# Kernel optimization log

Hardware: AMD Instinct MI355X
Metric: run time of the kernel (lower is better)

The kernel has to match this reference:

```python
import jax, jax.numpy as jnp
import numpy as np
import math

HIDDEN = 2048
HEADS = 16
HEAD_DIM = HIDDEN // HEADS
MAX_SEQ = 2048
BATCH = 2
SEQ = 2048


def _rope_tables(seq_len, dim):
    inv_freq = 1.0 / (10000.0 ** (np.arange(0, dim, 2, dtype=np.float32) / dim))
    t = np.arange(seq_len, dtype=np.float32)
    freqs = np.einsum('i,j->ij', t, inv_freq)  # [S, dim/2]
    emb = np.concatenate([freqs, freqs], axis=-1)  # [S, dim]
    return jnp.asarray(np.cos(emb)), jnp.asarray(np.sin(emb))


def setup_inputs() -> dict:
    key = jax.random.key(0)
    ks = jax.random.split(key, 5)
    s = 1.0 / math.sqrt(HIDDEN)
    x = jax.random.normal(ks[0], (BATCH, SEQ, HIDDEN), dtype=jnp.float32)
    Wq = jax.random.normal(ks[1], (HIDDEN, HIDDEN), dtype=jnp.float32) * s
    Wk = jax.random.normal(ks[2], (HIDDEN, HIDDEN), dtype=jnp.float32) * s
    Wv = jax.random.normal(ks[3], (HIDDEN, HIDDEN), dtype=jnp.float32) * s
    Wo = jax.random.normal(ks[4], (HIDDEN, HIDDEN), dtype=jnp.float32) * s
    return {"x": x, "Wq": Wq, "Wk": Wk, "Wv": Wv, "Wo": Wo}


def _rotate_half(t):
    t1, t2 = t[..., : t.shape[-1] // 2], t[..., t.shape[-1] // 2 :]
    return jnp.concatenate([-t2, t1], axis=-1)


def reference(x, Wq, Wk, Wv, Wo):
    b, s, _ = x.shape
    # nn.Linear: y = x @ W.T
    def proj(W):
        return jnp.einsum('bsd,hd->bsh', x, W).reshape(b, s, HEADS, HEAD_DIM).transpose(0, 2, 1, 3)
    q, k, v = proj(Wq), proj(Wk), proj(Wv)  # [b, H, s, hd]
    cos, sin = _rope_tables(s, HEAD_DIM)    # [s, hd]
    cos = cos[None, None]
    sin = sin[None, None]
    q = q * cos + _rotate_half(q) * sin
    k = k * cos + _rotate_half(k) * sin
    scale = 1.0 / math.sqrt(HEAD_DIM)
    scores = jnp.einsum('bhqd,bhkd->bhqk', q, k) * scale
    causal = jnp.triu(jnp.ones((s, s), dtype=bool), k=1)
    scores = jnp.where(causal[None, None], -jnp.inf, scores)
    attn = jax.nn.softmax(scores, axis=-1)
    out = jnp.einsum('bhqk,bhkd->bhqd', attn, v)
    out = out.transpose(0, 2, 1, 3).reshape(b, s, HIDDEN)
    return jnp.einsum('bsd,hd->bsh', out, Wo)
```

## Files before the change

### kernel.cpp

```cpp
#include <hip/hip_runtime.h>
#include <stdint.h>


#define SCALE_Q 0.08838834764831845f

typedef short bf16x8 __attribute__((ext_vector_type(8)));
typedef float f32x4 __attribute__((ext_vector_type(4)));
typedef unsigned short u16x4v __attribute__((ext_vector_type(4)));
typedef unsigned short u16x8v __attribute__((ext_vector_type(8)));

__device__ __forceinline__ unsigned short f2bf(float f) {
  unsigned u = __float_as_uint(f);
  return (unsigned short)((u + 0x7FFFu + ((u >> 16) & 1u)) >> 16);
}
__device__ __forceinline__ float bf2f(unsigned short h) {
  return __uint_as_float(((unsigned)h) << 16);
}
__device__ __forceinline__ void gld16(void* lds, const void* g) {
  __builtin_amdgcn_global_load_lds(
      (const __attribute__((address_space(1))) unsigned int*)g,
      (__attribute__((address_space(3))) unsigned int*)lds, 16, 0, 0);
}

__global__ __launch_bounds__(256) void cvt_all(
    const float* __restrict__ x, const float* __restrict__ wq,
    const float* __restrict__ wk, const float* __restrict__ wv,
    const float* __restrict__ wo,
    unsigned short* __restrict__ xb, unsigned short* __restrict__ wqkv,
    unsigned short* __restrict__ wob) {
  int r = blockIdx.y;
  size_t i = ((size_t)blockIdx.x * 256 + threadIdx.x) * 8;
  const float* src; unsigned short* dst; size_t n;
  if (r == 0)      { src = x;  dst = xb;             n = 8388608; }
  else if (r == 1) { src = wq; dst = wqkv;           n = 4194304; }
  else if (r == 2) { src = wk; dst = wqkv + 4194304; n = 4194304; }
  else if (r == 3) { src = wv; dst = wqkv + 8388608; n = 4194304; }
  else             { src = wo; dst = wob;            n = 4194304; }
  if (i >= n) return;
  float4 a = *(const float4*)(src + i);
  float4 b = *(const float4*)(src + i + 4);
  u16x8v o;
  o[0] = f2bf(a.x); o[1] = f2bf(a.y); o[2] = f2bf(a.z); o[3] = f2bf(a.w);
  o[4] = f2bf(b.x); o[5] = f2bf(b.y); o[6] = f2bf(b.z); o[7] = f2bf(b.w);
  *(u16x8v*)(dst + i) = o;
}

__global__ __launch_bounds__(256) void rope_table(float* __restrict__ ct, float* __restrict__ st) {
  int id = blockIdx.x * 256 + threadIdx.x;
  int s = id >> 6, j = id & 63;
  float inv = __powf(10000.0f, -(float)j * (1.0f / 64.0f));
  float a = (float)s * inv;
  ct[id] = __cosf(a);
  st[id] = __sinf(a);
}

template <int MODE>
__global__ __launch_bounds__(512, 2) void gemm8p(
    const unsigned short* __restrict__ A, const unsigned short* __restrict__ B,
    void* __restrict__ C0, void* __restrict__ C1, void* __restrict__ C2,
    int N, int Kd, int nbx) {
  __shared__ unsigned short As[4][128 * 64];
  __shared__ unsigned short Bs[4][128 * 64];
  const int t = threadIdx.x;
  const int lane = t & 63, w = t >> 6;
  const int g = lane >> 4, c15 = lane & 15;
  const int wm = w >> 2, wn = w & 3;

  const int chunk = (int)blockIdx.x & 7;
  const int idx = (int)blockIdx.x >> 3;
  const int cpc = nbx >> 3;
  const int row = idx & 15;
  const int col = chunk * cpc + (idx >> 4);
  const int brow = row * 256, bcol = col * 256;

  const int l = t >> 3;
  const int lg = (t & 7) ^ (l & 7);
  const unsigned short* srcA = A + (size_t)(brow + l + ((lg >> 2) << 7)) * Kd + (lg & 3) * 8;
  const unsigned short* srcB = B + (size_t)(bcol + l + ((lg >> 2) << 7)) * Kd + (lg & 3) * 8;

  auto stage = [&](int kt) {
    const int buf = kt & 3;
    const unsigned short* a = srcA + kt * 32;
    const unsigned short* b = srcB + kt * 32;
    gld16((char*)As[buf] + t * 16, a);
    gld16((char*)As[buf] + 8192 + t * 16, a + (size_t)64 * Kd);
    gld16((char*)Bs[buf] + t * 16, b);
    gld16((char*)Bs[buf] + 8192 + t * 16, b + (size_t)64 * Kd);
  };

  const int aoff = c15 * 128 + ((((wm << 2) | g) ^ (c15 & 7)) << 4);
  const int boff = ((wn & 1) << 13) + c15 * 128 + (((((wn >> 1) << 2) | g) ^ (c15 & 7)) << 4);

  f32x4 zero4 = {0.f, 0.f, 0.f, 0.f};
  f32x4 acc[8][4];
#pragma unroll
  for (int a_ = 0; a_ < 8; ++a_)
#pragma unroll
    for (int b_ = 0; b_ < 4; ++b_) acc[a_][b_] = zero4;

  const int nk = Kd >> 5;
  stage(0); stage(1); stage(2);
  asm volatile("s_waitcnt vmcnt(8)" ::: "memory");
  __builtin_amdgcn_s_barrier();

  for (int kt = 0; kt < nk; ++kt) {
    const char* ab = (const char*)As[kt & 3];
    const char* bb = (const char*)Bs[kt & 3];
    bf16x8 bfv[4], af0[4], af1[4];
#pragma unroll
    for (int nj = 0; nj < 4; ++nj) bfv[nj] = *(const bf16x8*)(bb + boff + nj * 2048);
#pragma unroll
    for (int mi = 0; mi < 4; ++mi) af0[mi] = *(const bf16x8*)(ab + aoff + mi * 2048);
    __builtin_amdgcn_sched_barrier(0);
#pragma unroll
    for (int mi = 0; mi < 4; ++mi) af1[mi] = *(const bf16x8*)(ab + aoff + (mi + 4) * 2048);
    if (kt + 3 < nk) stage(kt + 3);
    asm volatile("s_waitcnt lgkmcnt(4)" ::: "memory");
    __builtin_amdgcn_sched_barrier(0);
    __builtin_amdgcn_s_setprio(1);
#pragma unroll
    for (int mi = 0; mi < 4; ++mi)
#pragma unroll
      for (int nj = 0; nj < 4; ++nj)
        acc[mi][nj] = __builtin_amdgcn_mfma_f32_16x16x32_bf16(
            af0[mi], bfv[nj], acc[mi][nj], 0, 0, 0);
    __builtin_amdgcn_s_setprio(0);
    asm volatile("s_waitcnt lgkmcnt(0)" ::: "memory");
    __builtin_amdgcn_sched_barrier(0);
    __builtin_amdgcn_s_setprio(1);
#pragma unroll
    for (int mi = 0; mi < 4; ++mi)
#pragma unroll
      for (int nj = 0; nj < 4; ++nj)
        acc[mi + 4][nj] = __builtin_amdgcn_mfma_f32_16x16x32_bf16(
            af1[mi], bfv[nj], acc[mi + 4][nj], 0, 0, 0);
    __builtin_amdgcn_s_setprio(0);
    if (kt + 3 < nk) {
      asm volatile("s_waitcnt vmcnt(8)" ::: "memory");
    } else if (kt + 2 < nk) {
      asm volatile("s_waitcnt vmcnt(4)" ::: "memory");
    } else if (kt + 1 < nk) {
      asm volatile("s_waitcnt vmcnt(0)" ::: "memory");
    }
    __builtin_amdgcn_s_barrier();
  }

#pragma unroll
  for (int mi = 0; mi < 8; ++mi) {
#pragma unroll
    for (int nj = 0; nj < 4; ++nj) {
      f32x4 v = acc[mi][nj];
      int row0 = brow + wm * 128 + mi * 16 + g * 4;
      int colc = bcol + wn * 64 + nj * 16 + c15;
      if (MODE == 0) {
        int which = colc >> 11;
        int hc = colc & 2047;
        int bh = ((row0 >> 11) << 4) + (hc >> 7);
        int d = hc & 127, s0 = row0 & 2047;
        if (which == 2) {
          u16x4v pk;
          pk[0] = f2bf(v[0]); pk[1] = f2bf(v[1]); pk[2] = f2bf(v[2]); pk[3] = f2bf(v[3]);
          *(u16x4v*)((unsigned short*)C2 + ((size_t)bh * 128 + d) * 2048 + s0) = pk;
        } else {
          unsigned short* dst =
              (unsigned short*)(which ? C1 : C0) + ((size_t)bh * 2048 + s0) * 128 + d;
#pragma unroll
          for (int i = 0; i < 4; ++i) dst[(size_t)i * 128] = f2bf(v[i]);
        }
      } else {
        float* Cf = (float*)C0;
#pragma unroll
        for (int i = 0; i < 4; ++i) Cf[(size_t)(row0 + i) * N + colc] = v[i];
      }
    }
  }
}

__global__ __launch_bounds__(256) void rope_apply(
    unsigned short* __restrict__ Q, unsigned short* __restrict__ K,
    const float* __restrict__ ct, const float* __restrict__ st) {
  int id = blockIdx.x * 256 + threadIdx.x;
  int o = id & 7;
  int s = (id >> 3) & 2047;
  int bh = id >> 14;
  size_t base = ((size_t)bh * 2048 + s) * 128 + o * 8;
  u16x8v qlo = *(u16x8v*)(Q + base), qhi = *(u16x8v*)(Q + base + 64);
  u16x8v klo = *(u16x8v*)(K + base), khi = *(u16x8v*)(K + base + 64);
  const float* cp = ct + s * 64 + o * 8;
  const float* sp = st + s * 64 + o * 8;
#pragma unroll
  for (int j = 0; j < 8; ++j) {
    float c = cp[j], sn = sp[j];
    float ql = bf2f(qlo[j]), qh = bf2f(qhi[j]);
    qlo[j] = f2bf((ql * c - qh * sn) * SCALE_Q);
    qhi[j] = f2bf((qh * c + ql * sn) * SCALE_Q);
    float kl = bf2f(klo[j]), kh = bf2f(khi[j]);
    klo[j] = f2bf(kl * c - kh * sn);
    khi[j] = f2bf(kh * c + kl * sn);
  }
  *(u16x8v*)(Q + base) = qlo; *(u16x8v*)(Q + base + 64) = qhi;
  *(u16x8v*)(K + base) = klo; *(u16x8v*)(K + base + 64) = khi;
}

__global__ __launch_bounds__(256) void attn_fwd(
    const unsigned short* __restrict__ Qg, const unsigned short* __restrict__ Kg,
    const unsigned short* __restrict__ Vtg, unsigned short* __restrict__ Og) {
  __shared__ unsigned short Ks[2][64 * 128];
  __shared__ unsigned short Vs[2][64 * 128];
  __shared__ unsigned short Pl[4][16 * 88];
  const int t = threadIdx.x;
  const int lane = t & 63, w = t >> 6;
  const int g = lane >> 4, c15 = lane & 15;
  const int pair = blockIdx.x;
  const int bh = blockIdx.y;
  const int b = bh >> 4, h = bh & 15;

  const int ksrow = t >> 4;
  const int kssl = (t & 15) ^ ksrow;
  const unsigned short* kp = Kg + ((size_t)bh * 2048 + ksrow) * 128 + kssl * 8;
  const int vsrow = t >> 3;
  const int vssl = (t & 7) ^ (vsrow & 7);
  const unsigned short* vp = Vtg + ((size_t)bh * 128 + vsrow) * 2048 + vssl * 8;

  auto stageTile = [&](int buf, int tkv) {
#pragma unroll
    for (int c = 0; c < 4; ++c) {
      gld16((char*)Ks[buf] + c * 4096 + t * 16, kp + (size_t)(tkv * 64 + c * 16) * 128);
      gld16((char*)Vs[buf] + c * 4096 + t * 16, vp + (size_t)c * 32 * 2048 + tkv * 64);
    }
  };

  f32x4 zero4 = {0.f, 0.f, 0.f, 0.f};
  f32x4 o[8];
  float mrow[4], lrow[4];
  bf16x8 qf[4];

  auto computeTile = [&](int buf, int qb, int tkv) {
    const int q0 = qb * 64;
    const int qrow = q0 + w * 16;
    f32x4 sv[4];
    __builtin_amdgcn_s_setprio(1);
#pragma unroll
    for (int cb = 0; cb < 4; ++cb) {
      f32x4 z = zero4;
#pragma unroll
      for (int kf = 0; kf < 4; ++kf) {
        int row = cb * 16 + c15;
        int p = (kf * 4 + g) ^ c15;
        bf16x8 kfr = *(const bf16x8*)((const char*)Ks[buf] + row * 256 + p * 16);
        z = __builtin_amdgcn_mfma_f32_16x16x32_bf16(qf[kf], kfr, z, 0, 0, 0);
      }
      sv[cb] = z;
    }
    __builtin_amdgcn_s_setprio(0);
    if (tkv == qb) {
#pragma unroll
      for (int cb = 0; cb < 4; ++cb)
#pragma unroll
        for (int i = 0; i < 4; ++i) {
          int colk = q0 + cb * 16 + c15;
          int rq = qrow + g * 4 + i;
          if (colk > rq) sv[cb][i] = -1e30f;
        }
    }
    float pmx[4];
#pragma unroll
    for (int i = 0; i < 4; ++i)
      pmx[i] = fmaxf(fmaxf(sv[0][i], sv[1][i]), fmaxf(sv[2][i], sv[3][i]));
#pragma unroll
    for (int dd = 1; dd < 16; dd <<= 1)
#pragma unroll
      for (int i = 0; i < 4; ++i) pmx[i] = fmaxf(pmx[i], __shfl_xor(pmx[i], dd));
    float sc[4], psum[4];
#pragma unroll
    for (int i = 0; i < 4; ++i) {
      float nm = fmaxf(mrow[i], pmx[i]);
      sc[i] = __expf(mrow[i] - nm);
      mrow[i] = nm;
      psum[i] = 0.f;
    }
#pragma unroll
    for (int cb = 0; cb < 4; ++cb)
#pragma unroll
      for (int i = 0; i < 4; ++i) {
        float e = __expf(sv[cb][i] - mrow[i]);
        sv[cb][i] = e;
        psum[i] += e;
      }
#pragma unroll
    for (int dd = 1; dd < 16; dd <<= 1)
#pragma unroll
      for (int i = 0; i < 4; ++i) psum[i] += __shfl_xor(psum[i], dd);
#pragma unroll
    for (int i = 0; i < 4; ++i) lrow[i] = lrow[i] * sc[i] + psum[i];
#pragma unroll
    for (int db = 0; db < 8; ++db)
#pragma unroll
      for (int i = 0; i < 4; ++i) o[db][i] *= sc[i];

    unsigned short* pw = &Pl[w][0];
#pragma unroll
    for (int cb = 0; cb < 4; ++cb)
#pragma unroll
      for (int i = 0; i < 4; ++i)
        pw[(g * 4 + i) * 88 + cb * 16 + c15] = f2bf(sv[cb][i]);
    bf16x8 pf[2];
#pragma unroll
    for (int kb = 0; kb < 2; ++kb)
      pf[kb] = *(const bf16x8*)((const char*)pw + c15 * 176 + kb * 64 + g * 16);

    __builtin_amdgcn_s_setprio(1);
#pragma unroll
    for (int db = 0; db < 8; ++db) {
#pragma unroll
      for (int kb = 0; kb < 2; ++kb) {
        int row = db * 16 + c15;
        int p = (kb * 4 + g) ^ (c15 & 7);
        bf16x8 vfr = *(const bf16x8*)((const char*)Vs[buf] + row * 128 + p * 16);
        o[db] = __builtin_amdgcn_mfma_f32_16x16x32_bf16(pf[kb], vfr, o[db], 0, 0, 0);
      }
    }
    __builtin_amdgcn_s_setprio(0);
  };

  auto loadQ = [&](int qb) {
    const unsigned short* qp = Qg + ((size_t)bh * 2048 + qb * 64 + w * 16 + c15) * 128 + g * 8;
#pragma unroll
    for (int kf = 0; kf < 4; ++kf) qf[kf] = *(const bf16x8*)(qp + kf * 32);
#pragma unroll
    for (int db = 0; db < 8; ++db) o[db] = zero4;
#pragma unroll
    for (int i = 0; i < 4; ++i) { mrow[i] = -1e30f; lrow[i] = 0.f; }
  };

  auto writeO = [&](int qb) {
    float linv[4];
#pragma unroll
    for (int i = 0; i < 4; ++i) linv[i] = 1.0f / lrow[i];
#pragma unroll
    for (int db = 0; db < 8; ++db)
#pragma unroll
      for (int i = 0; i < 4; ++i) {
        int q = qb * 64 + w * 16 + g * 4 + i;
        Og[((size_t)(b * 2048 + q)) * 2048 + h * 128 + db * 16 + c15] =
            f2bf(o[db][i] * linv[i]);
      }
  };

  const int qbA = pair, qbB = 31 - pair;
  const int ntA = qbA + 1, ntB = qbB + 1;
  int cur = 0;

  stageTile(0, 0);
  loadQ(qbA);
  for (int tkv = 0; tkv < ntA; ++tkv) {
    __syncthreads();
    if (tkv + 1 < ntA) stageTile(cur ^ 1, tkv + 1);
    else               stageTile(cur ^ 1, 0);
    computeTile(cur, qbA, tkv);
    cur ^= 1;
  }
  writeO(qbA);
  loadQ(qbB);
  for (int tkv = 0; tkv < ntB; ++tkv) {
    __syncthreads();
    if (tkv + 1 < ntB) stageTile(cur ^ 1, tkv + 1);
    computeTile(cur, qbB, tkv);
    cur ^= 1;
  }
  writeO(qbB);
}

extern "C" void kernel_launch(void* const* d_in, const int* in_sizes, int n_in,
                              void* d_out, int out_size, void* d_ws, size_t ws_size,
                              hipStream_t stream) {
  const float* x  = (const float*)d_in[0];
  const float* Wq = (const float*)d_in[1];
  const float* Wk = (const float*)d_in[2];
  const float* Wv = (const float*)d_in[3];
  const float* Wo = (const float*)d_in[4];
  char* p = (char*)d_ws;
  unsigned short* xb    = (unsigned short*)p;
  unsigned short* wqkvb = (unsigned short*)(p + 16777216);
  unsigned short* wob   = (unsigned short*)(p + 41943040);
  unsigned short* Qb    = (unsigned short*)(p + 50331648);
  unsigned short* Kb    = (unsigned short*)(p + 67108864);
  unsigned short* Vt    = (unsigned short*)(p + 83886080);
  float* ctab           = (float*)(p + 100663296);
  float* stab           = (float*)(p + 101187584);
  unsigned short* Ao = xb;

  cvt_all<<<dim3(4096, 5), 256, 0, stream>>>(x, Wq, Wk, Wv, Wo, xb, wqkvb, wob);
  rope_table<<<512, 256, 0, stream>>>(ctab, stab);
  gemm8p<0><<<384, 512, 0, stream>>>(xb, wqkvb, Qb, Kb, Vt, 6144, 2048, 24);
  rope_apply<<<2048, 256, 0, stream>>>(Qb, Kb, ctab, stab);
  attn_fwd<<<dim3(16, 32), 256, 0, stream>>>(Qb, Kb, Vt, Ao);
  gemm8p<1><<<128, 512, 0, stream>>>(Ao, wob, d_out, nullptr, nullptr, 2048, 2048, 8);
}
```

Measured before the change: 303.5 us.

## Restructure GEMM into double-buffered K=64 ping-pong pipeline with interleaved staging

Replaces the 4-stage K=32 LDS ring in the projection GEMMs with a 2-buffer K=64 scheme. Global-to-LDS loads are split into quarter-tile components that are issued between MFMA clusters, with barriers and priority toggles fencing each phase. The goal is to hide global-load and LDS-read latency behind matrix math with fewer loop iterations. The cost is many extra workgroup barriers per iteration and tighter buffer reuse, which could stall warps. The remaining edits only rename variables and add macros.

Result: slower. 318.6 us (+5.0%).

```diff
diff --git a/kernel.cpp b/kernel.cpp
--- a/kernel.cpp
+++ b/kernel.cpp
@@ -21,6 +21,14 @@
       (const __attribute__((address_space(1))) unsigned int*)g,
       (__attribute__((address_space(3))) unsigned int*)lds, 16, 0, 0);
 }
+
+#define BAR __builtin_amdgcn_s_barrier()
+#define SB0 __builtin_amdgcn_sched_barrier(0)
+#define LGKM0 asm volatile("s_waitcnt lgkmcnt(0)" ::: "memory")
+#define VM4 asm volatile("s_waitcnt vmcnt(4)" ::: "memory")
+#define VM0 asm volatile("s_waitcnt vmcnt(0)" ::: "memory")
+#define PRIO1 __builtin_amdgcn_s_setprio(1)
+#define PRIO0 __builtin_amdgcn_s_setprio(0)
 
 __global__ __launch_bounds__(256) void cvt_all(
     const float* __restrict__ x, const float* __restrict__ wq,
@@ -55,12 +63,12 @@
 }
 
 template <int MODE>
-__global__ __launch_bounds__(512, 2) void gemm8p(
+__global__ __launch_bounds__(512, 2) void gemm_m2(
     const unsigned short* __restrict__ A, const unsigned short* __restrict__ B,
     void* __restrict__ C0, void* __restrict__ C1, void* __restrict__ C2,
     int N, int Kd, int nbx) {
-  __shared__ unsigned short As[4][128 * 64];
-  __shared__ unsigned short Bs[4][128 * 64];
+  __shared__ unsigned short As[2][256 * 64];
+  __shared__ unsigned short Bs[2][256 * 64];
   const int t = threadIdx.x;
   const int lane = t & 63, w = t >> 6;
   const int g = lane >> 4, c15 = lane & 15;
@@ -73,23 +81,27 @@
   const int col = chunk * cpc + (idx >> 4);
   const int brow = row * 256, bcol = col * 256;
 
-  const int l = t >> 3;
-  const int lg = (t & 7) ^ (l & 7);
-  const unsigned short* srcA = A + (size_t)(brow + l + ((lg >> 2) << 7)) * Kd + (lg & 3) * 8;
-  const unsigned short* srcB = B + (size_t)(bcol + l + ((lg >> 2) << 7)) * Kd + (lg & 3) * 8;
-
-  auto stage = [&](int kt) {
-    const int buf = kt & 3;
-    const unsigned short* a = srcA + kt * 32;
-    const unsigned short* b = srcB + kt * 32;
-    gld16((char*)As[buf] + t * 16, a);
-    gld16((char*)As[buf] + 8192 + t * 16, a + (size_t)64 * Kd);
-    gld16((char*)Bs[buf] + t * 16, b);
-    gld16((char*)Bs[buf] + 8192 + t * 16, b + (size_t)64 * Kd);
-  };
-
-  const int aoff = c15 * 128 + ((((wm << 2) | g) ^ (c15 & 7)) << 4);
-  const int boff = ((wn & 1) << 13) + c15 * 128 + (((((wn >> 1) << 2) | g) ^ (c15 & 7)) << 4);
+  const int r8 = t >> 3;
+  const int lg = (t & 7) ^ (r8 & 7);
+  const unsigned short* srcA = A + (size_t)(brow + r8) * Kd + lg * 8;
+  const unsigned short* srcB = B + (size_t)(bcol + r8) * Kd + lg * 8;
+
+  const int nk = Kd >> 6;
+  const int nit = nk >> 1;
+
+  auto stage = [&](int step, int comp) {
+    if (step >= nk) return;
+    char* dst = ((comp & 2) ? (char*)Bs[step & 1] : (char*)As[step & 1]) + (comp & 1) * 16384;
+    const unsigned short* src =
+        ((comp & 2) ? srcB : srcA) + (size_t)((comp & 1) * 128) * Kd + step * 64;
+    gld16(dst + t * 16, src);
+    gld16(dst + 8192 + t * 16, src + (size_t)64 * Kd);
+  };
+
+  const int aBase = (wm * 128 + c15) * 128;
+  const int bBase = (wn * 64 + c15) * 128;
+  const int sl0 = ((g) ^ (c15 & 7)) * 16;
+  const int sl1 = ((4 + g) ^ (c15 & 7)) * 16;
 
   f32x4 zero4 = {0.f, 0.f, 0.f, 0.f};
   f32x4 acc[8][4];
@@ -98,51 +110,66 @@
 #pragma unroll
     for (int b_ = 0; b_ < 4; ++b_) acc[a_][b_] = zero4;
 
-  const int nk = Kd >> 5;
-  stage(0); stage(1); stage(2);
-  asm volatile("s_waitcnt vmcnt(8)" ::: "memory");
-  __builtin_amdgcn_s_barrier();
-
-  for (int kt = 0; kt < nk; ++kt) {
-    const char* ab = (const char*)As[kt & 3];
-    const char* bb = (const char*)Bs[kt & 3];
-    bf16x8 bfv[4], af0[4], af1[4];
-#pragma unroll
-    for (int nj = 0; nj < 4; ++nj) bfv[nj] = *(const bf16x8*)(bb + boff + nj * 2048);
-#pragma unroll
-    for (int mi = 0; mi < 4; ++mi) af0[mi] = *(const bf16x8*)(ab + aoff + mi * 2048);
-    __builtin_amdgcn_sched_barrier(0);
-#pragma unroll
-    for (int mi = 0; mi < 4; ++mi) af1[mi] = *(const bf16x8*)(ab + aoff + (mi + 4) * 2048);
-    if (kt + 3 < nk) stage(kt + 3);
-    asm volatile("s_waitcnt lgkmcnt(4)" ::: "memory");
-    __builtin_amdgcn_sched_barrier(0);
-    __builtin_amdgcn_s_setprio(1);
+  bf16x8 af0[8], bf0[4], af1[8], bf1[4];
+
+  auto RD = [&](const char* ab, const char* bb, bf16x8* AF, bf16x8* BF, int sl) {
+#pragma unroll
+    for (int mi = 0; mi < 8; ++mi) AF[mi] = *(const bf16x8*)(ab + aBase + mi * 2048 + sl);
+#pragma unroll
+    for (int nj = 0; nj < 4; ++nj) BF[nj] = *(const bf16x8*)(bb + bBase + nj * 2048 + sl);
+  };
+  auto MF16 = [&](const bf16x8* AF, const bf16x8* BF, int mb) {
 #pragma unroll
     for (int mi = 0; mi < 4; ++mi)
 #pragma unroll
       for (int nj = 0; nj < 4; ++nj)
-        acc[mi][nj] = __builtin_amdgcn_mfma_f32_16x16x32_bf16(
-            af0[mi], bfv[nj], acc[mi][nj], 0, 0, 0);
-    __builtin_amdgcn_s_setprio(0);
-    asm volatile("s_waitcnt lgkmcnt(0)" ::: "memory");
-    __builtin_amdgcn_sched_barrier(0);
-    __builtin_amdgcn_s_setprio(1);
-#pragma unroll
-    for (int mi = 0; mi < 4; ++mi)
-#pragma unroll
-      for (int nj = 0; nj < 4; ++nj)
-        acc[mi + 4][nj] = __builtin_amdgcn_mfma_f32_16x16x32_bf16(
-            af1[mi], bfv[nj], acc[mi + 4][nj], 0, 0, 0);
-    __builtin_amdgcn_s_setprio(0);
-    if (kt + 3 < nk) {
-      asm volatile("s_waitcnt vmcnt(8)" ::: "memory");
-    } else if (kt + 2 < nk) {
-      asm volatile("s_waitcnt vmcnt(4)" ::: "memory");
-    } else if (kt + 1 < nk) {
-      asm volatile("s_waitcnt vmcnt(0)" ::: "memory");
-    }
-    __builtin_amdgcn_s_barrier();
+        acc[mb + mi][nj] = __builtin_amdgcn_mfma_f32_16x16x32_bf16(
+            AF[mb + mi], BF[nj], acc[mb + mi][nj], 0, 0, 0);
+  };
+
+  stage(0, 0); stage(0, 1); stage(0, 2); stage(0, 3);
+  stage(1, 0); stage(1, 1);
+  VM4;
+  BAR; SB0;
+
+  for (int i = 0; i < nit; ++i) {
+    const char* a0 = (const char*)As[0]; const char* b0 = (const char*)Bs[0];
+    const char* a1 = (const char*)As[1]; const char* b1 = (const char*)Bs[1];
+    const int sB = 2 * i + 1, sN = 2 * i + 2, sN1 = 2 * i + 3;
+    RD(a0, b0, af0, bf0, sl0); stage(sB, 2);
+    BAR; LGKM0; SB0;
+    PRIO1; MF16(af0, bf0, 0); PRIO0;
+    BAR; SB0;
+    RD(a0, b0, af1, bf1, sl1); stage(sB, 3);
+    BAR; LGKM0; SB0;
+    PRIO1; MF16(af0, bf0, 4); PRIO0;
+    BAR; SB0;
+    stage(sN, 0);
+    BAR; SB0;
+    PRIO1; MF16(af1, bf1, 0); PRIO0;
+    BAR; SB0;
+    stage(sN, 1);
+    BAR; SB0;
+    PRIO1; MF16(af1, bf1, 4); PRIO0;
+    if (i + 1 == nit) { VM0; } else { VM4; }
+    BAR; SB0;
+    RD(a1, b1, af0, bf0, sl0); stage(sN, 2);
+    BAR; LGKM0; SB0;
+    PRIO1; MF16(af0, bf0, 0); PRIO0;
+    BAR; SB0;
+    RD(a1, b1, af1, bf1, sl1); stage(sN, 3);
+    BAR; LGKM0; SB0;
+    PRIO1; MF16(af0, bf0, 4); PRIO0;
+    BAR; SB0;
+    stage(sN1, 0);
+    BAR; SB0;
+    PRIO1; MF16(af1, bf1, 0); PRIO0;
+    BAR; SB0;
+    stage(sN1, 1);
+    BAR; SB0;
+    PRIO1; MF16(af1, bf1, 4); PRIO0;
+    VM4;
+    BAR; SB0;
   }
 
 #pragma unroll
@@ -165,12 +192,12 @@
           unsigned short* dst =
               (unsigned short*)(which ? C1 : C0) + ((size_t)bh * 2048 + s0) * 128 + d;
 #pragma unroll
-          for (int i = 0; i < 4; ++i) dst[(size_t)i * 128] = f2bf(v[i]);
+          for (int i2 = 0; i2 < 4; ++i2) dst[(size_t)i2 * 128] = f2bf(v[i2]);
         }
       } else {
         float* Cf = (float*)C0;
 #pragma unroll
-        for (int i = 0; i < 4; ++i) Cf[(size_t)(row0 + i) * N + colc] = v[i];
+        for (int i2 = 0; i2 < 4; ++i2) Cf[(size_t)(row0 + i2) * N + colc] = v[i2];
       }
     }
   }
@@ -239,20 +266,20 @@
     const int q0 = qb * 64;
     const int qrow = q0 + w * 16;
     f32x4 sv[4];
-    __builtin_amdgcn_s_setprio(1);
+    PRIO1;
 #pragma unroll
     for (int cb = 0; cb < 4; ++cb) {
       f32x4 z = zero4;
 #pragma unroll
       for (int kf = 0; kf < 4; ++kf) {
-        int row = cb * 16 + c15;
+        int rowk = cb * 16 + c15;
         int p = (kf * 4 + g) ^ c15;
-        bf16x8 kfr = *(const bf16x8*)((const char*)Ks[buf] + row * 256 + p * 16);
+        bf16x8 kfr = *(const bf16x8*)((const char*)Ks[buf] + rowk * 256 + p * 16);
         z = __builtin_amdgcn_mfma_f32_16x16x32_bf16(qf[kf], kfr, z, 0, 0, 0);
       }
       sv[cb] = z;
     }
-    __builtin_amdgcn_s_setprio(0);
+    PRIO0;
     if (tkv == qb) {
 #pragma unroll
       for (int cb = 0; cb < 4; ++cb)
@@ -309,18 +336,18 @@
     for (int kb = 0; kb < 2; ++kb)
       pf[kb] = *(const bf16x8*)((const char*)pw + c15 * 176 + kb * 64 + g * 16);
 
-    __builtin_amdgcn_s_setprio(1);
+    PRIO1;
 #pragma unroll
     for (int db = 0; db < 8; ++db) {
 #pragma unroll
       for (int kb = 0; kb < 2; ++kb) {
-        int row = db * 16 + c15;
+        int rowv = db * 16 + c15;
         int p = (kb * 4 + g) ^ (c15 & 7);
-        bf16x8 vfr = *(const bf16x8*)((const char*)Vs[buf] + row * 128 + p * 16);
+        bf16x8 vfr = *(const bf16x8*)((const char*)Vs[buf] + rowv * 128 + p * 16);
         o[db] = __builtin_amdgcn_mfma_f32_16x16x32_bf16(pf[kb], vfr, o[db], 0, 0, 0);
       }
     }
-    __builtin_amdgcn_s_setprio(0);
+    PRIO0;
   };
 
   auto loadQ = [&](int qb) {
@@ -392,8 +419,8 @@
 
   cvt_all<<<dim3(4096, 5), 256, 0, stream>>>(x, Wq, Wk, Wv, Wo, xb, wqkvb, wob);
   rope_table<<<512, 256, 0, stream>>>(ctab, stab);
-  gemm8p<0><<<384, 512, 0, stream>>>(xb, wqkvb, Qb, Kb, Vt, 6144, 2048, 24);
+  gemm_m2<0><<<384, 512, 0, stream>>>(xb, wqkvb, Qb, Kb, Vt, 6144, 2048, 24);
   rope_apply<<<2048, 256, 0, stream>>>(Qb, Kb, ctab, stab);
   attn_fwd<<<dim3(16, 32), 256, 0, stream>>>(Qb, Kb, Vt, Ao);
-  gemm8p<1><<<128, 512, 0, stream>>>(Ao, wob, d_out, nullptr, nullptr, 2048, 2048, 8);
-}
+  gemm_m2<1><<<128, 512, 0, stream>>>(Ao, wob, d_out, nullptr, nullptr, 2048, 2048, 8);
+}
```

## Shrink QKV GEMM to double buffering and use simpler 128x128 GEMM for output

Applied to the files above, without the earlier changes.

The QKV projection GEMM goes from a 4-stage to a 2-stage LDS pipeline, prefetching one tile ahead with a full vmcnt(0) wait each iteration. Halving LDS use may allow more resident blocks. The output projection now runs in a new single-buffered 128x128-tile kernel with 256 threads and 512 blocks instead of 128 large 256x256 blocks, meant to improve CU occupancy on that smaller GEMM. The cost is less latency hiding: loads are no longer overlapped with compute in the new kernel, and the QKV GEMM has a shallower prefetch.

Result: faster. 297.1 us (-2.1%).

```diff
diff --git a/kernel.cpp b/kernel.cpp
--- a/kernel.cpp
+++ b/kernel.cpp
@@ -54,13 +54,12 @@
   st[id] = __sinf(a);
 }
 
-template <int MODE>
-__global__ __launch_bounds__(512, 2) void gemm8p(
+__global__ __launch_bounds__(512, 2) void gemm8p2(
     const unsigned short* __restrict__ A, const unsigned short* __restrict__ B,
     void* __restrict__ C0, void* __restrict__ C1, void* __restrict__ C2,
     int N, int Kd, int nbx) {
-  __shared__ unsigned short As[4][128 * 64];
-  __shared__ unsigned short Bs[4][128 * 64];
+  __shared__ unsigned short As[2][128 * 64];
+  __shared__ unsigned short Bs[2][128 * 64];
   const int t = threadIdx.x;
   const int lane = t & 63, w = t >> 6;
   const int g = lane >> 4, c15 = lane & 15;
@@ -79,7 +78,7 @@
   const unsigned short* srcB = B + (size_t)(bcol + l + ((lg >> 2) << 7)) * Kd + (lg & 3) * 8;
 
   auto stage = [&](int kt) {
-    const int buf = kt & 3;
+    const int buf = kt & 1;
     const unsigned short* a = srcA + kt * 32;
     const unsigned short* b = srcB + kt * 32;
     gld16((char*)As[buf] + t * 16, a);
@@ -99,13 +98,13 @@
     for (int b_ = 0; b_ < 4; ++b_) acc[a_][b_] = zero4;
 
   const int nk = Kd >> 5;
-  stage(0); stage(1); stage(2);
-  asm volatile("s_waitcnt vmcnt(8)" ::: "memory");
+  stage(0);
+  asm volatile("s_waitcnt vmcnt(0)" ::: "memory");
   __builtin_amdgcn_s_barrier();
 
   for (int kt = 0; kt < nk; ++kt) {
-    const char* ab = (const char*)As[kt & 3];
-    const char* bb = (const char*)Bs[kt & 3];
+    const char* ab = (const char*)As[kt & 1];
+    const char* bb = (const char*)Bs[kt & 1];
     bf16x8 bfv[4], af0[4], af1[4];
 #pragma unroll
     for (int nj = 0; nj < 4; ++nj) bfv[nj] = *(const bf16x8*)(bb + boff + nj * 2048);
@@ -114,7 +113,7 @@
     __builtin_amdgcn_sched_barrier(0);
 #pragma unroll
     for (int mi = 0; mi < 4; ++mi) af1[mi] = *(const bf16x8*)(ab + aoff + (mi + 4) * 2048);
-    if (kt + 3 < nk) stage(kt + 3);
+    if (kt + 1 < nk) stage(kt + 1);
     asm volatile("s_waitcnt lgkmcnt(4)" ::: "memory");
     __builtin_amdgcn_sched_barrier(0);
     __builtin_amdgcn_s_setprio(1);
@@ -135,13 +134,7 @@
         acc[mi + 4][nj] = __builtin_amdgcn_mfma_f32_16x16x32_bf16(
             af1[mi], bfv[nj], acc[mi + 4][nj], 0, 0, 0);
     __builtin_amdgcn_s_setprio(0);
-    if (kt + 3 < nk) {
-      asm volatile("s_waitcnt vmcnt(8)" ::: "memory");
-    } else if (kt + 2 < nk) {
-      asm volatile("s_waitcnt vmcnt(4)" ::: "memory");
-    } else if (kt + 1 < nk) {
-      asm volatile("s_waitcnt vmcnt(0)" ::: "memory");
-    }
+    asm volatile("s_waitcnt vmcnt(0)" ::: "memory");
     __builtin_amdgcn_s_barrier();
   }
 
@@ -152,28 +145,95 @@
       f32x4 v = acc[mi][nj];
       int row0 = brow + wm * 128 + mi * 16 + g * 4;
       int colc = bcol + wn * 64 + nj * 16 + c15;
-      if (MODE == 0) {
-        int which = colc >> 11;
-        int hc = colc & 2047;
-        int bh = ((row0 >> 11) << 4) + (hc >> 7);
-        int d = hc & 127, s0 = row0 & 2047;
-        if (which == 2) {
-          u16x4v pk;
-          pk[0] = f2bf(v[0]); pk[1] = f2bf(v[1]); pk[2] = f2bf(v[2]); pk[3] = f2bf(v[3]);
-          *(u16x4v*)((unsigned short*)C2 + ((size_t)bh * 128 + d) * 2048 + s0) = pk;
-        } else {
-          unsigned short* dst =
-              (unsigned short*)(which ? C1 : C0) + ((size_t)bh * 2048 + s0) * 128 + d;
-#pragma unroll
-          for (int i = 0; i < 4; ++i) dst[(size_t)i * 128] = f2bf(v[i]);
-        }
+      int which = colc >> 11;
+      int hc = colc & 2047;
+      int bh = ((row0 >> 11) << 4) + (hc >> 7);
+      int d = hc & 127, s0 = row0 & 2047;
+      if (which == 2) {
+        u16x4v pk;
+        pk[0] = f2bf(v[0]); pk[1] = f2bf(v[1]); pk[2] = f2bf(v[2]); pk[3] = f2bf(v[3]);
+        *(u16x4v*)((unsigned short*)C2 + ((size_t)bh * 128 + d) * 2048 + s0) = pk;
       } else {
-        float* Cf = (float*)C0;
-#pragma unroll
-        for (int i = 0; i < 4; ++i) Cf[(size_t)(row0 + i) * N + colc] = v[i];
-      }
-    }
-  }
+        unsigned short* dst =
+            (unsigned short*)(which ? C1 : C0) + ((size_t)bh * 2048 + s0) * 128 + d;
+#pragma unroll
+        for (int i2 = 0; i2 < 4; ++i2) dst[(size_t)i2 * 128] = f2bf(v[i2]);
+      }
+    }
+  }
+}
+
+__global__ __launch_bounds__(256) void gemm_bt(
+    const unsigned short* __restrict__ A, const unsigned short* __restrict__ B,
+    float* __restrict__ C, int N, int Kd) {
+  __shared__ unsigned short As[128 * 64];
+  __shared__ unsigned short Bs[128 * 64];
+  const int t = threadIdx.x;
+  const int lane = t & 63, w = t >> 6;
+  const int g = lane >> 4, c15 = lane & 15;
+  const int wr = w >> 1, wc = w & 1;
+  const int brow = blockIdx.y * 128, bcol = blockIdx.x * 128;
+  const int srow = t >> 3;
+  const int ssl = (t & 7) ^ (srow & 7);
+  const unsigned short* pA = A + (size_t)(brow + srow) * Kd + ssl * 8;
+  const unsigned short* pB = B + (size_t)(bcol + srow) * Kd + ssl * 8;
+
+  int aoff[4][2], boff[4][2];
+#pragma unroll
+  for (int mi = 0; mi < 4; ++mi)
+#pragma unroll
+    for (int kk = 0; kk < 2; ++kk) {
+      int arow = wr * 64 + mi * 16 + c15;
+      int bcolr = wc * 64 + mi * 16 + c15;
+      int p = (kk * 4 + g) ^ (c15 & 7);
+      aoff[mi][kk] = arow * 128 + (p << 4);
+      boff[mi][kk] = bcolr * 128 + (p << 4);
+    }
+  f32x4 zero4 = {0.f, 0.f, 0.f, 0.f};
+  f32x4 acc[4][4];
+#pragma unroll
+  for (int a_ = 0; a_ < 4; ++a_)
+#pragma unroll
+    for (int b_ = 0; b_ < 4; ++b_) acc[a_][b_] = zero4;
+
+  const int nk = Kd >> 6;
+  for (int kt = 0; kt < nk; ++kt) {
+    const unsigned short* a0 = pA + kt * 64;
+    const unsigned short* b0 = pB + kt * 64;
+#pragma unroll
+    for (int c = 0; c < 4; ++c) {
+      gld16((char*)As + c * 4096 + t * 16, a0 + (size_t)c * 32 * Kd);
+      gld16((char*)Bs + c * 4096 + t * 16, b0 + (size_t)c * 32 * Kd);
+    }
+    __syncthreads();
+    bf16x8 af[4][2], bfv[4][2];
+#pragma unroll
+    for (int mi = 0; mi < 4; ++mi)
+#pragma unroll
+      for (int kk = 0; kk < 2; ++kk) {
+        af[mi][kk] = *(const bf16x8*)((const char*)As + aoff[mi][kk]);
+        bfv[mi][kk] = *(const bf16x8*)((const char*)Bs + boff[mi][kk]);
+      }
+#pragma unroll
+    for (int mi = 0; mi < 4; ++mi)
+#pragma unroll
+      for (int nj = 0; nj < 4; ++nj)
+#pragma unroll
+        for (int kk = 0; kk < 2; ++kk)
+          acc[mi][nj] = __builtin_amdgcn_mfma_f32_16x16x32_bf16(
+              af[mi][kk], bfv[nj][kk], acc[mi][nj], 0, 0, 0);
+    __syncthreads();
+  }
+#pragma unroll
+  for (int mi = 0; mi < 4; ++mi)
+#pragma unroll
+    for (int nj = 0; nj < 4; ++nj) {
+      f32x4 v = acc[mi][nj];
+      int row0 = brow + wr * 64 + mi * 16 + g * 4;
+      int colc = bcol + wc * 64 + nj * 16 + c15;
+#pragma unroll
+      for (int i = 0; i < 4; ++i) C[(size_t)(row0 + i) * N + colc] = v[i];
+    }
 }
 
 __global__ __launch_bounds__(256) void rope_apply(
@@ -245,9 +305,9 @@
       f32x4 z = zero4;
 #pragma unroll
       for (int kf = 0; kf < 4; ++kf) {
-        int row = cb * 16 + c15;
+        int rowk = cb * 16 + c15;
         int p = (kf * 4 + g) ^ c15;
-        bf16x8 kfr = *(const bf16x8*)((const char*)Ks[buf] + row * 256 + p * 16);
+        bf16x8 kfr = *(const bf16x8*)((const char*)Ks[buf] + rowk * 256 + p * 16);
         z = __builtin_amdgcn_mfma_f32_16x16x32_bf16(qf[kf], kfr, z, 0, 0, 0);
       }
       sv[cb] = z;
@@ -314,9 +374,9 @@
     for (int db = 0; db < 8; ++db) {
 #pragma unroll
       for (int kb = 0; kb < 2; ++kb) {
-        int row = db * 16 + c15;
+        int rowv = db * 16 + c15;
         int p = (kb * 4 + g) ^ (c15 & 7);
-        bf16x8 vfr = *(const bf16x8*)((const char*)Vs[buf] + row * 128 + p * 16);
+        bf16x8 vfr = *(const bf16x8*)((const char*)Vs[buf] + rowv * 128 + p * 16);
         o[db] = __builtin_amdgcn_mfma_f32_16x16x32_bf16(pf[kb], vfr, o[db], 0, 0, 0);
       }
     }
@@ -392,8 +452,8 @@
 
   cvt_all<<<dim3(4096, 5), 256, 0, stream>>>(x, Wq, Wk, Wv, Wo, xb, wqkvb, wob);
   rope_table<<<512, 256, 0, stream>>>(ctab, stab);
-  gemm8p<0><<<384, 512, 0, stream>>>(xb, wqkvb, Qb, Kb, Vt, 6144, 2048, 24);
+  gemm8p2<<<384, 512, 0, stream>>>(xb, wqkvb, Qb, Kb, Vt, 6144, 2048, 24);
   rope_apply<<<2048, 256, 0, stream>>>(Qb, Kb, ctab, stab);
   attn_fwd<<<dim3(16, 32), 256, 0, stream>>>(Qb, Kb, Vt, Ao);
-  gemm8p<1><<<128, 512, 0, stream>>>(Ao, wob, d_out, nullptr, nullptr, 2048, 2048, 8);
-}
+  gemm_bt<<<dim3(16, 32), 256, 0, stream>>>(Ao, wob, (float*)d_out, 2048, 2048);
+}
```
